# Kernel tuning notes

Hardware: AMD Instinct MI355X
Metric: run time of the kernel (lower is better)

## Reference

```python
import jax
import jax.numpy as jnp
from jax import lax
import numpy as np

# module hyperparameters (match init_kwargs)
IN_C, OUT_C = 32, 64
K, STRIDE, PAD, DIL = 3, 1, 1, 1
GRID_SIZE, ORDER = 5, 3
GRID_LO, GRID_HI = -1.0, 1.0
SCALE_SPLINE = 1.0
EPS = 1e-8


def _knot_grid():
    # grid = arange(-order, grid_size+order+1) * h + lo ; length = grid_size + 2*order + 1 = 12
    h = (GRID_HI - GRID_LO) / GRID_SIZE
    return jnp.arange(-ORDER, GRID_SIZE + ORDER + 1, dtype=jnp.float32) * h + GRID_LO


def _bspline_bases(x):
    """Cox-de Boor recursion. x: (N, P) -> bases: (N, P, GRID_SIZE+ORDER)."""
    grid = _knot_grid()
    xe = x[..., None]  # (N, P, 1)
    bases = ((xe >= grid[:-1]) & (xe < grid[1:])).astype(x.dtype)  # (N, P, 11)
    for k in range(1, ORDER + 1):
        left_den = jnp.maximum(grid[k:-1] - grid[:-(k + 1)], EPS)
        right_den = jnp.maximum(grid[k + 1:] - grid[1:-k], EPS)
        bases = ((xe - grid[:-(k + 1)]) / left_den * bases[..., :-1]
                 + (grid[k + 1:] - xe) / right_den * bases[..., 1:])
    return bases  # (N, P, 8)


def setup_inputs() -> dict:
    key = jax.random.key(0)
    k1, k2, k3 = jax.random.split(key, 3)
    x = jax.random.normal(k1, (4, IN_C, 56, 56), dtype=jnp.float32)
    base_weight = jax.random.normal(k2, (OUT_C, IN_C, K, K), dtype=jnp.float32) * 0.05
    spline_weight = jax.random.normal(k3, (OUT_C, IN_C * K * K, GRID_SIZE + ORDER), dtype=jnp.float32) * 0.05
    spline_scaler = jnp.ones((OUT_C,), dtype=jnp.float32)
    return {"x": x, "base_weight": base_weight,
            "spline_weight": spline_weight, "spline_scaler": spline_scaler}


def reference(x, base_weight, spline_weight, spline_scaler):
    B, C, H, W = x.shape
    pad = [(PAD, PAD), (PAD, PAD)]
    # base path: conv2d -> SiLU
    base_conv = lax.conv_general_dilated(
        x, base_weight, window_strides=(STRIDE, STRIDE), padding=pad,
        rhs_dilation=(DIL, DIL), dimension_numbers=("NCHW", "OIHW", "NCHW"))
    base_out = jax.nn.silu(base_conv)

    # unfold: (B, C*K*K, oh, ow) with torch Unfold channel ordering (c, kh, kw)
    patches = lax.conv_general_dilated_patches(
        x, filter_shape=(K, K), window_strides=(STRIDE, STRIDE), padding=pad,
        rhs_dilation=(DIL, DIL))
    oh, ow = patches.shape[2], patches.shape[3]
    num_patches = oh * ow
    # (B*num_patches, C*K*K)
    pf = patches.reshape(B, C * K * K, num_patches).transpose(0, 2, 1).reshape(-1, C * K * K)

    bases = _bspline_bases(pf)  # (N, P, F)
    # contract patch-dim and basis-dim against spline weights
    spl = jnp.einsum("npf,opf->no", bases, spline_weight) * spline_scaler  # (N, O)
    spl = spl.reshape(B, num_patches, OUT_C).transpose(0, 2, 1).reshape(B, OUT_C, oh, ow)
    return base_out + SCALE_SPLINE * spl
```

## Files before the change

### kernel.cpp

```cpp
#include <hip/hip_runtime.h>
#include <math.h>


typedef __attribute__((ext_vector_type(8))) short bf16x8;
typedef __attribute__((ext_vector_type(4))) float f32x4;

#define MFMA16(a, b, c) __builtin_amdgcn_mfma_f32_16x16x32_bf16((a), (b), (c), 0, 0, 0)

__device__ __forceinline__ unsigned short f2bf(float f) {
    unsigned u = __builtin_bit_cast(unsigned, f);
    u = (u + 0x7fffu + ((u >> 16) & 1u)) >> 16;
    return (unsigned short)u;
}

__device__ __forceinline__ void eval_bases(float v, float bs[8]) {
    #pragma unroll
    for (int i = 0; i < 8; ++i) bs[i] = 0.0f;
    float t = (v + 2.2f) * 2.5f;
    if (t >= 0.0f && t < 11.0f) {
        int j = (int)t;
        if (j > 10) j = 10;
        float knot = (float)(j - 3) * 0.4f - 1.0f;
        float u  = (v - knot) * 2.5f;
        float um = 1.0f - u;
        float u2 = u * u, u3 = u2 * u;
        const float s6 = 1.0f / 6.0f;
        float w0 = um * um * um * s6;
        float w1 = (3.0f * u3 - 6.0f * u2 + 4.0f) * s6;
        float w2 = (-3.0f * u3 + 3.0f * u2 + 3.0f * u + 1.0f) * s6;
        float w3 = u3 * s6;
        int i0 = j - 3;
        if (i0 >= 0)               bs[i0]     = w0;
        if (i0 + 1 >= 0 && i0 < 7) bs[i0 + 1] = w1;
        if (i0 + 2 >= 0 && i0 < 6) bs[i0 + 2] = w2;
        if (i0 + 3 <= 7)           bs[i0 + 3] = w3;
    }
}

__global__ __launch_bounds__(256)
void cvt_swz_kernel(const float* __restrict__ ws, const float* __restrict__ wb,
                    unsigned short* __restrict__ wst, unsigned short* __restrict__ wbt) {
    int i = blockIdx.x * 256 + threadIdx.x;
    if (i < 147456) {
        int j = i & 7, l = (i >> 3) & 63, t = i >> 9;
        int S = t % 72, nq = t / 72;
        int oc = nq * 16 + (l & 15);
        int k  = S * 32 + (l >> 4) * 8 + j;
        wst[i] = f2bf(ws[oc * 2304 + k]);
    } else {
        int i2 = i - 147456;
        if (i2 < 18432) {
            int j = i2 & 7, l = (i2 >> 3) & 63, t = i2 >> 9;
            int s = t % 9, nq = t / 9;
            int oc = nq * 16 + (l & 15);
            int c  = (l >> 4) * 8 + j;
            wbt[i2] = f2bf(wb[oc * 288 + c * 9 + s]);
        }
    }
}

__global__ __launch_bounds__(512)
void kan_mfma_kernel(const float* __restrict__ x,
                     const float* __restrict__ sc,
                     const unsigned short* __restrict__ wst,
                     const unsigned short* __restrict__ wbt,
                     float* __restrict__ out) {
    __shared__ unsigned short smem[29600];
    unsigned short* sb = smem;
    unsigned short* xh = smem + 25600;

    const int tid = threadIdx.x;
    const int bx  = blockIdx.x;
    const int b   = bx / 49;
    const int r   = bx - b * 49;
    const int ty  = r / 7;
    const int tx  = r - ty * 7;
    const int h0  = ty * 8, w0 = tx * 8;

    const int lane = tid & 63;
    const int wv   = tid >> 6;
    const int nq   = wv & 3;
    const int kh   = wv >> 2;
    const int ml   = lane & 15;
    const int kg   = lane >> 4;
    const int py0  = ml >> 3, px0 = ml & 7;

    float vv[7];
    #pragma unroll
    for (int j = 0; j < 7; ++j) {
        int i = tid + j * 512;
        float val = 0.0f;
        if (i < 3200) {
            int c  = i / 100;
            int hp = i - c * 100;
            int hy = hp / 10;
            int hx = hp - hy * 10;
            int hh = h0 + hy - 1, ww = w0 + hx - 1;
            if ((unsigned)hh < 56u && (unsigned)ww < 56u)
                val = x[((b * 32 + c) * 56 + hh) * 56 + ww];
        }
        vv[j] = val;
    }
    #pragma unroll
    for (int j = 0; j < 7; ++j) {
        int i = tid + j * 512;
        if (i < 3200) {
            int c  = i / 100;
            int hp = i - c * 100;
            float bs[8];
            eval_bases(vv[j], bs);
            bf16x8 pk;
            #pragma unroll
            for (int j2 = 0; j2 < 8; ++j2) pk[j2] = (short)f2bf(bs[j2]);
            *reinterpret_cast<bf16x8*>(&sb[i * 8]) = pk;
            xh[hp * 40 + c] = f2bf(vv[j]);
        }
    }
    __syncthreads();

    int aoff[9];
    #pragma unroll
    for (int u = 0; u < 9; ++u) {
        int tt  = 4 * u + kg;
        int dc  = tt / 9;
        int tap = tt - dc * 9;
        int th  = tap / 3;
        int tw  = tap - th * 3;
        aoff[u] = (dc * 100 + (py0 + th) * 10 + (px0 + tw)) * 8;
    }

    f32x4 aS[4] = {{0,0,0,0},{0,0,0,0},{0,0,0,0},{0,0,0,0}};
    f32x4 aB[4] = {{0,0,0,0},{0,0,0,0},{0,0,0,0},{0,0,0,0}};

    const unsigned short* bp = wst + ((nq * 72 + kh * 36) * 64 + lane) * 8;
    int cbase = kh * 12800;
    for (int g = 0; g < 4; ++g) {
        #pragma unroll
        for (int u = 0; u < 9; ++u) {
            bf16x8 bw = *reinterpret_cast<const bf16x8*>(bp + (g * 9 + u) * 512);
            #pragma unroll
            for (int f = 0; f < 4; ++f) {
                bf16x8 a = *reinterpret_cast<const bf16x8*>(&sb[cbase + aoff[u] + f * 160]);
                aS[f] = MFMA16(a, bw, aS[f]);
            }
        }
        cbase += 3200;
    }

    {
        const unsigned short* bbp = wbt + (nq * 9 * 64 + lane) * 8;
        const int sbeg = kh ? 5 : 0;
        const int send = kh ? 9 : 5;
        for (int s = sbeg; s < send; ++s) {
            int th = (s * 11) >> 5;
            int tw = s - 3 * th;
            bf16x8 bw = *reinterpret_cast<const bf16x8*>(bbp + s * 512);
            int xa = ((py0 + th) * 10 + (px0 + tw)) * 40 + kg * 8;
            #pragma unroll
            for (int f = 0; f < 4; ++f) {
                bf16x8 a = *reinterpret_cast<const bf16x8*>(&xh[xa + f * 800]);
                aB[f] = MFMA16(a, bw, aB[f]);
            }
        }
    }

    __syncthreads();
    float* red = reinterpret_cast<float*>(smem);
    const int idx = nq * 64 + lane;
    if (kh) {
        #pragma unroll
        for (int f = 0; f < 4; ++f)
            #pragma unroll
            for (int w = 0; w < 4; ++w) red[(f * 4 + w) * 260 + idx] = aS[f][w];
        #pragma unroll
        for (int f = 0; f < 4; ++f)
            #pragma unroll
            for (int w = 0; w < 4; ++w) red[((16 + f * 4) + w) * 260 + idx] = aB[f][w];
    }
    __syncthreads();
    if (!kh) {
        #pragma unroll
        for (int f = 0; f < 4; ++f)
            #pragma unroll
            for (int w = 0; w < 4; ++w) aS[f][w] += red[(f * 4 + w) * 260 + idx];
        #pragma unroll
        for (int f = 0; f < 4; ++f)
            #pragma unroll
            for (int w = 0; w < 4; ++w) aB[f][w] += red[((16 + f * 4) + w) * 260 + idx];

        const int oc  = nq * 16 + ml;
        const float scv = sc[oc];
        #pragma unroll
        for (int f = 0; f < 4; ++f) {
            const int py  = f * 2 + (kg >> 1);
            const int pxb = (kg & 1) * 4;
            float* ob = out + ((b * 64 + oc) * 56 + h0 + py) * 56 + w0 + pxb;
            f32x4 res;
            #pragma unroll
            for (int reg = 0; reg < 4; ++reg) {
                float bv = aB[f][reg];
                float si = bv / (1.0f + __expf(-bv));
                res[reg] = si + scv * aS[f][reg];
            }
            *reinterpret_cast<f32x4*>(ob) = res;
        }
    }
}

extern "C" void kernel_launch(void* const* d_in, const int* in_sizes, int n_in,
                              void* d_out, int out_size, void* d_ws, size_t ws_size,
                              hipStream_t stream) {
    const float* x  = (const float*)d_in[0];
    const float* wb = (const float*)d_in[1];
    const float* ws = (const float*)d_in[2];
    const float* sc = (const float*)d_in[3];
    float* out = (float*)d_out;

    unsigned short* wst = (unsigned short*)d_ws;
    unsigned short* wbt = wst + 147456;

    cvt_swz_kernel<<<648, 256, 0, stream>>>(ws, wb, wst, wbt);
    kan_mfma_kernel<<<196, 512, 0, stream>>>(x, sc, wst, wbt, out);
}
```

Measured before the change: 73.17 us.

## Switch to 32x32x16 MFMA tiles with 4-way K-split across waves

```diff
diff --git a/kernel.cpp b/kernel.cpp
--- a/kernel.cpp
+++ b/kernel.cpp
@@ -4,8 +4,9 @@
 
 typedef __attribute__((ext_vector_type(8))) short bf16x8;
 typedef __attribute__((ext_vector_type(4))) float f32x4;
-
-#define MFMA16(a, b, c) __builtin_amdgcn_mfma_f32_16x16x32_bf16((a), (b), (c), 0, 0, 0)
+typedef __attribute__((ext_vector_type(16))) float f32x16;
+
+#define MFMA32(a, b, c) __builtin_amdgcn_mfma_f32_32x32x16_bf16((a), (b), (c), 0, 0, 0)
 
 __device__ __forceinline__ unsigned short f2bf(float f) {
     unsigned u = __builtin_bit_cast(unsigned, f);
@@ -42,19 +43,20 @@
                     unsigned short* __restrict__ wst, unsigned short* __restrict__ wbt) {
     int i = blockIdx.x * 256 + threadIdx.x;
     if (i < 147456) {
-        int j = i & 7, l = (i >> 3) & 63, t = i >> 9;
-        int S = t % 72, nq = t / 72;
-        int oc = nq * 16 + (l & 15);
-        int k  = S * 32 + (l >> 4) * 8 + j;
+        int j = i & 7, l = (i >> 3) & 63, tq = i >> 9;
+        int t = tq % 144, nqq = tq / 144;
+        int oc = nqq * 32 + (l & 31);
+        int k  = t * 16 + (l >> 5) * 8 + j;
         wst[i] = f2bf(ws[oc * 2304 + k]);
     } else {
         int i2 = i - 147456;
         if (i2 < 18432) {
-            int j = i2 & 7, l = (i2 >> 3) & 63, t = i2 >> 9;
-            int s = t % 9, nq = t / 9;
-            int oc = nq * 16 + (l & 15);
-            int c  = (l >> 4) * 8 + j;
-            wbt[i2] = f2bf(wb[oc * 288 + c * 9 + s]);
+            int j = i2 & 7, l = (i2 >> 3) & 63, tq = i2 >> 9;
+            int t = tq % 18, nqq = tq / 18;
+            int oc  = nqq * 32 + (l & 31);
+            int tap = t >> 1;
+            int c   = 16 * (t & 1) + (l >> 5) * 8 + j;
+            wbt[i2] = f2bf(wb[oc * 288 + c * 9 + tap]);
         }
     }
 }
@@ -79,11 +81,11 @@
 
     const int lane = tid & 63;
     const int wv   = tid >> 6;
-    const int nq   = wv & 3;
-    const int kh   = wv >> 2;
-    const int ml   = lane & 15;
-    const int kg   = lane >> 4;
-    const int py0  = ml >> 3, px0 = ml & 7;
+    const int nqq  = wv & 1;
+    const int kq   = wv >> 1;
+    const int hl   = lane >> 5;
+    const int rl   = lane & 31;
+    const int py   = rl >> 3, px = rl & 7;
 
     float vv[7];
     #pragma unroll
@@ -118,91 +120,89 @@
     }
     __syncthreads();
 
-    int aoff[9];
+    int aoff2[9];
     #pragma unroll
     for (int u = 0; u < 9; ++u) {
-        int tt  = 4 * u + kg;
-        int dc  = tt / 9;
-        int tap = tt - dc * 9;
+        int tt  = 2 * u + hl;
+        int dc  = tt >= 9 ? 1 : 0;
+        int tap = tt - 9 * dc;
         int th  = tap / 3;
         int tw  = tap - th * 3;
-        aoff[u] = (dc * 100 + (py0 + th) * 10 + (px0 + tw)) * 8;
-    }
-
-    f32x4 aS[4] = {{0,0,0,0},{0,0,0,0},{0,0,0,0},{0,0,0,0}};
-    f32x4 aB[4] = {{0,0,0,0},{0,0,0,0},{0,0,0,0},{0,0,0,0}};
-
-    const unsigned short* bp = wst + ((nq * 72 + kh * 36) * 64 + lane) * 8;
-    int cbase = kh * 12800;
-    for (int g = 0; g < 4; ++g) {
+        aoff2[u] = (dc * 100 + (py + th) * 10 + (px + tw)) * 8;
+    }
+
+    f32x16 accS0 = {0,0,0,0,0,0,0,0,0,0,0,0,0,0,0,0};
+    f32x16 accS1 = {0,0,0,0,0,0,0,0,0,0,0,0,0,0,0,0};
+
+    const unsigned short* bp = wst + ((nqq * 144 + kq * 36) * 64 + lane) * 8;
+    for (int a = 0; a < 4; ++a) {
+        const int cbase = (kq * 8 + 2 * a) * 800;
         #pragma unroll
         for (int u = 0; u < 9; ++u) {
-            bf16x8 bw = *reinterpret_cast<const bf16x8*>(bp + (g * 9 + u) * 512);
-            #pragma unroll
-            for (int f = 0; f < 4; ++f) {
-                bf16x8 a = *reinterpret_cast<const bf16x8*>(&sb[cbase + aoff[u] + f * 160]);
-                aS[f] = MFMA16(a, bw, aS[f]);
-            }
-        }
-        cbase += 3200;
-    }
-
-    {
-        const unsigned short* bbp = wbt + (nq * 9 * 64 + lane) * 8;
-        const int sbeg = kh ? 5 : 0;
-        const int send = kh ? 9 : 5;
-        for (int s = sbeg; s < send; ++s) {
-            int th = (s * 11) >> 5;
-            int tw = s - 3 * th;
-            bf16x8 bw = *reinterpret_cast<const bf16x8*>(bbp + s * 512);
-            int xa = ((py0 + th) * 10 + (px0 + tw)) * 40 + kg * 8;
-            #pragma unroll
-            for (int f = 0; f < 4; ++f) {
-                bf16x8 a = *reinterpret_cast<const bf16x8*>(&xh[xa + f * 800]);
-                aB[f] = MFMA16(a, bw, aB[f]);
-            }
+            bf16x8 bw = *reinterpret_cast<const bf16x8*>(bp + (a * 9 + u) * 512);
+            bf16x8 a0 = *reinterpret_cast<const bf16x8*>(&sb[cbase + aoff2[u]]);
+            bf16x8 a1 = *reinterpret_cast<const bf16x8*>(&sb[cbase + aoff2[u] + 320]);
+            accS0 = MFMA32(a0, bw, accS0);
+            accS1 = MFMA32(a1, bw, accS1);
+        }
+    }
+
+    f32x16 accB0 = {0,0,0,0,0,0,0,0,0,0,0,0,0,0,0,0};
+    f32x16 accB1 = {0,0,0,0,0,0,0,0,0,0,0,0,0,0,0,0};
+    if (kq == 0) {
+        const unsigned short* bbp = wbt + (nqq * 18 * 64 + lane) * 8;
+        const int c0 = hl * 8;
+        #pragma unroll
+        for (int t = 0; t < 18; ++t) {
+            const int tap = t >> 1, th = tap / 3, tw = tap - 3 * th;
+            bf16x8 bw = *reinterpret_cast<const bf16x8*>(bbp + t * 512);
+            int xa = ((py + th) * 10 + (px + tw)) * 40 + 16 * (t & 1) + c0;
+            bf16x8 a0 = *reinterpret_cast<const bf16x8*>(&xh[xa]);
+            bf16x8 a1 = *reinterpret_cast<const bf16x8*>(&xh[xa + 1600]);
+            accB0 = MFMA32(a0, bw, accB0);
+            accB1 = MFMA32(a1, bw, accB1);
         }
     }
 
     __syncthreads();
     float* red = reinterpret_cast<float*>(smem);
-    const int idx = nq * 64 + lane;
-    if (kh) {
-        #pragma unroll
-        for (int f = 0; f < 4; ++f)
-            #pragma unroll
-            for (int w = 0; w < 4; ++w) red[(f * 4 + w) * 260 + idx] = aS[f][w];
-        #pragma unroll
-        for (int f = 0; f < 4; ++f)
-            #pragma unroll
-            for (int w = 0; w < 4; ++w) red[((16 + f * 4) + w) * 260 + idx] = aB[f][w];
+    const int col = nqq * 64 + lane;
+    if (kq) {
+        const int rb = (kq - 1) * 4096;
+        #pragma unroll
+        for (int w = 0; w < 16; ++w) red[rb + w * 128 + col] = accS0[w];
+        #pragma unroll
+        for (int w = 0; w < 16; ++w) red[rb + (16 + w) * 128 + col] = accS1[w];
     }
     __syncthreads();
-    if (!kh) {
-        #pragma unroll
-        for (int f = 0; f < 4; ++f)
-            #pragma unroll
-            for (int w = 0; w < 4; ++w) aS[f][w] += red[(f * 4 + w) * 260 + idx];
-        #pragma unroll
-        for (int f = 0; f < 4; ++f)
-            #pragma unroll
-            for (int w = 0; w < 4; ++w) aB[f][w] += red[((16 + f * 4) + w) * 260 + idx];
-
-        const int oc  = nq * 16 + ml;
+    if (kq == 0) {
+        #pragma unroll
+        for (int rr = 0; rr < 3; ++rr) {
+            const int rb = rr * 4096;
+            #pragma unroll
+            for (int w = 0; w < 16; ++w) accS0[w] += red[rb + w * 128 + col];
+            #pragma unroll
+            for (int w = 0; w < 16; ++w) accS1[w] += red[rb + (16 + w) * 128 + col];
+        }
+
+        const int oc  = nqq * 32 + rl;
         const float scv = sc[oc];
         #pragma unroll
-        for (int f = 0; f < 4; ++f) {
-            const int py  = f * 2 + (kg >> 1);
-            const int pxb = (kg & 1) * 4;
-            float* ob = out + ((b * 64 + oc) * 56 + h0 + py) * 56 + w0 + pxb;
-            f32x4 res;
-            #pragma unroll
-            for (int reg = 0; reg < 4; ++reg) {
-                float bv = aB[f][reg];
-                float si = bv / (1.0f + __expf(-bv));
-                res[reg] = si + scv * aS[f][reg];
+        for (int mq = 0; mq < 2; ++mq) {
+            f32x16 aS = mq ? accS1 : accS0;
+            f32x16 aB = mq ? accB1 : accB0;
+            #pragma unroll
+            for (int q = 0; q < 4; ++q) {
+                float* ob = out + ((b * 64 + oc) * 56 + h0 + mq * 4 + q) * 56 + w0 + 4 * hl;
+                f32x4 res;
+                #pragma unroll
+                for (int rr = 0; rr < 4; ++rr) {
+                    float bv = aB[q * 4 + rr];
+                    float si = bv / (1.0f + __expf(-bv));
+                    res[rr] = si + scv * aS[q * 4 + rr];
+                }
+                *reinterpret_cast<f32x4*>(ob) = res;
             }
-            *reinterpret_cast<f32x4*>(ob) = res;
         }
     }
 }
```

Result: slower. 76.83 us (+5.0%).

## Fuse weight bf16 conversion into main kernel with register-prefetched fp32 weights

Applied to the files above, without the earlier changes.

```diff
diff --git a/kernel.cpp b/kernel.cpp
--- a/kernel.cpp
+++ b/kernel.cpp
@@ -3,6 +3,7 @@
 
 
 typedef __attribute__((ext_vector_type(8))) short bf16x8;
+typedef __attribute__((ext_vector_type(8))) float f32x8;
 typedef __attribute__((ext_vector_type(4))) float f32x4;
 
 #define MFMA16(a, b, c) __builtin_amdgcn_mfma_f32_16x16x32_bf16((a), (b), (c), 0, 0, 0)
@@ -11,6 +12,13 @@
     unsigned u = __builtin_bit_cast(unsigned, f);
     u = (u + 0x7fffu + ((u >> 16) & 1u)) >> 16;
     return (unsigned short)u;
+}
+
+__device__ __forceinline__ bf16x8 cvt8(f32x8 w) {
+    bf16x8 r;
+    #pragma unroll
+    for (int j = 0; j < 8; ++j) r[j] = (short)f2bf(w[j]);
+    return r;
 }
 
 __device__ __forceinline__ void eval_bases(float v, float bs[8]) {
@@ -37,33 +45,11 @@
     }
 }
 
-__global__ __launch_bounds__(256)
-void cvt_swz_kernel(const float* __restrict__ ws, const float* __restrict__ wb,
-                    unsigned short* __restrict__ wst, unsigned short* __restrict__ wbt) {
-    int i = blockIdx.x * 256 + threadIdx.x;
-    if (i < 147456) {
-        int j = i & 7, l = (i >> 3) & 63, t = i >> 9;
-        int S = t % 72, nq = t / 72;
-        int oc = nq * 16 + (l & 15);
-        int k  = S * 32 + (l >> 4) * 8 + j;
-        wst[i] = f2bf(ws[oc * 2304 + k]);
-    } else {
-        int i2 = i - 147456;
-        if (i2 < 18432) {
-            int j = i2 & 7, l = (i2 >> 3) & 63, t = i2 >> 9;
-            int s = t % 9, nq = t / 9;
-            int oc = nq * 16 + (l & 15);
-            int c  = (l >> 4) * 8 + j;
-            wbt[i2] = f2bf(wb[oc * 288 + c * 9 + s]);
-        }
-    }
-}
-
-__global__ __launch_bounds__(512)
+__global__ __launch_bounds__(512, 2)
 void kan_mfma_kernel(const float* __restrict__ x,
+                     const float* __restrict__ wb,
+                     const float* __restrict__ ws,
                      const float* __restrict__ sc,
-                     const unsigned short* __restrict__ wst,
-                     const unsigned short* __restrict__ wbt,
                      float* __restrict__ out) {
     __shared__ unsigned short smem[29600];
     unsigned short* sb = smem;
@@ -80,10 +66,12 @@
     const int lane = tid & 63;
     const int wv   = tid >> 6;
     const int nq   = wv & 3;
-    const int kh   = wv >> 2;
+    const int kh   = wv >> 1 & 0;
+    const int khh  = wv >> 2;
     const int ml   = lane & 15;
     const int kg   = lane >> 4;
     const int py0  = ml >> 3, px0 = ml & 7;
+    (void)kh;
 
     float vv[7];
     #pragma unroll
@@ -101,6 +89,23 @@
         }
         vv[j] = val;
     }
+
+    const int s0  = khh ? 5 : 0;
+    const int nST = khh ? 4 : 5;
+    const float* wbsrc = wb + (nq * 16 + ml) * 288 + kg * 72 + s0;
+    float wbp[5][8];
+    #pragma unroll
+    for (int s = 0; s < 5; ++s)
+        if (s < nST) {
+            #pragma unroll
+            for (int j = 0; j < 8; ++j) wbp[s][j] = wbsrc[j * 9 + s];
+        }
+
+    const float* wsrc = ws + (nq * 16 + ml) * 2304 + khh * 36 * 32 + kg * 8;
+    f32x8 pw0 = *reinterpret_cast<const f32x8*>(wsrc);
+    f32x8 pw1 = *reinterpret_cast<const f32x8*>(wsrc + 32);
+    f32x8 pw2 = *reinterpret_cast<const f32x8*>(wsrc + 64);
+
     #pragma unroll
     for (int j = 0; j < 7; ++j) {
         int i = tid + j * 512;
@@ -132,61 +137,75 @@
     f32x4 aS[4] = {{0,0,0,0},{0,0,0,0},{0,0,0,0},{0,0,0,0}};
     f32x4 aB[4] = {{0,0,0,0},{0,0,0,0},{0,0,0,0},{0,0,0,0}};
 
-    const unsigned short* bp = wst + ((nq * 72 + kh * 36) * 64 + lane) * 8;
-    int cbase = kh * 12800;
-    for (int g = 0; g < 4; ++g) {
-        #pragma unroll
-        for (int u = 0; u < 9; ++u) {
-            bf16x8 bw = *reinterpret_cast<const bf16x8*>(bp + (g * 9 + u) * 512);
-            #pragma unroll
-            for (int f = 0; f < 4; ++f) {
-                bf16x8 a = *reinterpret_cast<const bf16x8*>(&sb[cbase + aoff[u] + f * 160]);
-                aS[f] = MFMA16(a, bw, aS[f]);
-            }
-        }
-        cbase += 3200;
-    }
-
-    {
-        const unsigned short* bbp = wbt + (nq * 9 * 64 + lane) * 8;
-        const int sbeg = kh ? 5 : 0;
-        const int send = kh ? 9 : 5;
-        for (int s = sbeg; s < send; ++s) {
-            int th = (s * 11) >> 5;
-            int tw = s - 3 * th;
-            bf16x8 bw = *reinterpret_cast<const bf16x8*>(bbp + s * 512);
-            int xa = ((py0 + th) * 10 + (px0 + tw)) * 40 + kg * 8;
+    const int kbase = khh * 12800;
+#define SPL_STEP(S, WREG) do {                                                   \
+        bf16x8 bwv = cvt8(WREG);                                                 \
+        if ((S) + 3 < 36)                                                        \
+            WREG = *reinterpret_cast<const f32x8*>(wsrc + ((S) + 3) * 32);       \
+        const int g_ = (S) / 9, u_ = (S) % 9;                                    \
+        const int ab = kbase + g_ * 3200;                                        \
+        bf16x8 a0 = *reinterpret_cast<const bf16x8*>(&sb[ab + aoff[u_]]);        \
+        bf16x8 a1 = *reinterpret_cast<const bf16x8*>(&sb[ab + aoff[u_] + 160]);  \
+        bf16x8 a2 = *reinterpret_cast<const bf16x8*>(&sb[ab + aoff[u_] + 320]);  \
+        bf16x8 a3 = *reinterpret_cast<const bf16x8*>(&sb[ab + aoff[u_] + 480]);  \
+        aS[0] = MFMA16(a0, bwv, aS[0]);                                          \
+        aS[1] = MFMA16(a1, bwv, aS[1]);                                          \
+        aS[2] = MFMA16(a2, bwv, aS[2]);                                          \
+        aS[3] = MFMA16(a3, bwv, aS[3]);                                          \
+    } while (0)
+
+    #pragma unroll
+    for (int Sb = 0; Sb < 36; Sb += 3) {
+        SPL_STEP(Sb + 0, pw0);
+        SPL_STEP(Sb + 1, pw1);
+        SPL_STEP(Sb + 2, pw2);
+    }
+#undef SPL_STEP
+
+    #pragma unroll
+    for (int s = 0; s < 5; ++s)
+        if (s < nST) {
+            const int tap = s0 + s;
+            const int th  = tap >= 6 ? 2 : (tap >= 3 ? 1 : 0);
+            const int tw  = tap - 3 * th;
+            bf16x8 bwv;
+            #pragma unroll
+            for (int j = 0; j < 8; ++j) bwv[j] = (short)f2bf(wbp[s][j]);
+            const int xa = ((py0 + th) * 10 + (px0 + tw)) * 40 + kg * 8;
             #pragma unroll
             for (int f = 0; f < 4; ++f) {
                 bf16x8 a = *reinterpret_cast<const bf16x8*>(&xh[xa + f * 800]);
-                aB[f] = MFMA16(a, bw, aB[f]);
+                aB[f] = MFMA16(a, bwv, aB[f]);
             }
         }
-    }
 
     __syncthreads();
     float* red = reinterpret_cast<float*>(smem);
     const int idx = nq * 64 + lane;
-    if (kh) {
-        #pragma unroll
-        for (int f = 0; f < 4; ++f)
+    if (khh) {
+        #pragma unroll
+        for (int f = 0; f < 4; ++f) {
             #pragma unroll
             for (int w = 0; w < 4; ++w) red[(f * 4 + w) * 260 + idx] = aS[f][w];
-        #pragma unroll
-        for (int f = 0; f < 4; ++f)
+        }
+        #pragma unroll
+        for (int f = 0; f < 4; ++f) {
             #pragma unroll
             for (int w = 0; w < 4; ++w) red[((16 + f * 4) + w) * 260 + idx] = aB[f][w];
+        }
     }
     __syncthreads();
-    if (!kh) {
-        #pragma unroll
-        for (int f = 0; f < 4; ++f)
+    if (!khh) {
+        #pragma unroll
+        for (int f = 0; f < 4; ++f) {
             #pragma unroll
             for (int w = 0; w < 4; ++w) aS[f][w] += red[(f * 4 + w) * 260 + idx];
-        #pragma unroll
-        for (int f = 0; f < 4; ++f)
+        }
+        #pragma unroll
+        for (int f = 0; f < 4; ++f) {
             #pragma unroll
             for (int w = 0; w < 4; ++w) aB[f][w] += red[((16 + f * 4) + w) * 260 + idx];
+        }
 
         const int oc  = nq * 16 + ml;
         const float scv = sc[oc];
@@ -216,9 +235,5 @@
     const float* sc = (const float*)d_in[3];
     float* out = (float*)d_out;
 
-    unsigned short* wst = (unsigned short*)d_ws;
-    unsigned short* wbt = wst + 147456;
-
-    cvt_swz_kernel<<<648, 256, 0, stream>>>(ws, wb, wst, wbt);
-    kan_mfma_kernel<<<196, 512, 0, stream>>>(x, sc, wst, wbt, out);
-}
+    kan_mfma_kernel<<<196, 512, 0, stream>>>(x, wb, ws, sc, out);
+}
```

Result: slower. 85.20 us (+16.4%).
